# Performance work log

Measured on AMD Instinct MI355X. Metric: run time of the kernel, lower is better.

## Reference

```python
import jax, jax.numpy as jnp
import numpy as np

N_LABELS = 2048
N_CLASSES = 2
BATCH = 2048
BRANCH = 4


def _tree():
    # deterministic rooted tree: parent(i) = (i-1)//BRANCH, node 0 is root
    parent = np.full(N_LABELS, -1, dtype=np.int64)
    parent[1:] = (np.arange(1, N_LABELS) - 1) // BRANCH
    depth = np.zeros(N_LABELS, dtype=np.int64)
    for i in range(1, N_LABELS):
        depth[i] = depth[parent[i]] + 1
    levels = [np.where(depth == d)[0] for d in range(int(depth.max()) + 1)]
    return parent, levels

_PARENT, _LEVELS = _tree()  # static structure (from the adjacency init arg)


def setup_inputs() -> dict:
    key = jax.random.key(0)
    k1, k2 = jax.random.split(key)
    emissions = jax.random.normal(k1, (BATCH, N_CLASSES, N_LABELS), dtype=jnp.float32)
    pairs = jax.random.normal(k2, (N_LABELS, N_LABELS, N_CLASSES, N_CLASSES), dtype=jnp.float32)
    return {"emissions": emissions, "pairs": pairs}


def _messages(emissions, pairs, upward):
    """Belief-propagation messages, level-synchronous (topological order).

    upward=True  -> alphas: messages from children to parents (leaves->root)
    upward=False -> betas:  messages from parents to children (root->leaves)
    """
    B, C, L = emissions.shape
    acc = jnp.zeros((B, C, L), emissions.dtype)
    if upward:
        # process deepest level first; all nodes at level d send to their
        # (level d-1) parents; duplicate parent indices accumulate via .add
        for d in range(len(_LEVELS) - 1, 0, -1):
            nodes = _LEVELS[d]      # senders (children), (K,)
            par = _PARENT[nodes]    # receivers (parents), (K,)
            # local[b, k, yc] = emissions[b, yc, node_k] + acc[b, yc, node_k]
            local = (emissions[:, :, nodes] + acc[:, :, nodes]).transpose(0, 2, 1)
            trans = pairs[par, nodes]  # (K, Cp, Cc): pairs[parent, child]
            # msg[b, k, yp] = logsumexp_yc( trans[k, yp, yc] + local[b, k, yc] )
            msg = jax.nn.logsumexp(trans[None] + local[:, :, None, :], axis=-1)
            acc = acc.at[:, :, par].add(msg.transpose(0, 2, 1))
    else:
        # process shallow -> deep; each node receives from its parent,
        # whose betas were completed in the previous level iteration
        for d in range(1, len(_LEVELS)):
            nodes = _LEVELS[d]      # receivers (children)
            par = _PARENT[nodes]    # senders (parents)
            local = (emissions[:, :, par] + acc[:, :, par]).transpose(0, 2, 1)  # (B,K,Cp)
            trans = pairs[nodes, par]  # (K, Cc, Cp): pairs[child, parent]
            msg = jax.nn.logsumexp(trans[None] + local[:, :, None, :], axis=-1)  # (B,K,Cc)
            acc = acc.at[:, :, nodes].add(msg.transpose(0, 2, 1))
    return acc


def reference(emissions, pairs):
    alphas = _messages(emissions, pairs, True)
    betas = _messages(emissions, pairs, False)
    scores = emissions + alphas + betas  # (B, C, L)
    # normalize over classes per label -> log marginals log p(y_i | X)
    return scores - jax.nn.logsumexp(scores, axis=1, keepdims=True)
```

## Files before the change

### kernel.cpp

```cpp
#include <hip/hip_runtime.h>


constexpr int NLAB = 2048;
constexpr int NBATCH = 2048;

#define LOG2E 1.4426950408889634f
#define LN2   0.6931471805599453f

__device__ __forceinline__ float fexp2(float x) { return __builtin_amdgcn_exp2f(x); }
__device__ __forceinline__ float flog2(float x) { return __builtin_amdgcn_logf(x); }

__global__ __launch_bounds__(256) void compact_pairs(
    const float4* __restrict__ pairs4,
    float4* __restrict__ up,
    float4* __restrict__ down)
{
    int i = blockIdx.x * 256 + threadIdx.x;
    if (i < NLAB - 1) {
        int c = i + 1, p = i >> 2;
        float4 t = pairs4[(size_t)p * NLAB + c];
        up[i] = make_float4(t.x, t.z,
                            fexp2((t.y - t.x) * LOG2E),
                            fexp2((t.w - t.z) * LOG2E));
        float4 s = pairs4[(size_t)c * NLAB + p];
        down[i] = make_float4(s.x, s.z,
                              fexp2((s.y - s.x) * LOG2E),
                              fexp2((s.w - s.z) * LOG2E));
    }
}

__global__ __launch_bounds__(256) void treecrf_kernel(
    const float* __restrict__ em_g,
    const float4* __restrict__ up,
    const float4* __restrict__ down,
    float* __restrict__ out)
{
    __shared__ float em[2 * NLAB];
    __shared__ float al[2 * NLAB];

    const int b = blockIdx.x;
    const int tid = threadIdx.x;
    const float* __restrict__ eb = em_g + (size_t)b * 2 * NLAB;

    for (int l2 = tid; l2 < NLAB / 2; l2 += 256) {
        float2 e0 = reinterpret_cast<const float2*>(eb)[l2];
        float2 e1 = reinterpret_cast<const float2*>(eb + NLAB)[l2];
        reinterpret_cast<float4*>(em)[l2] = make_float4(e0.x, e1.x, e0.y, e1.y);
        reinterpret_cast<float4*>(al)[l2] = make_float4(0.f, 0.f, 0.f, 0.f);
    }
    __syncthreads();

    const int ustart[6] = {1364, 340, 84, 20, 4, 0};
    const int uend[6]   = {2048, 1364, 340, 84, 20, 4};
#pragma unroll
    for (int pass = 0; pass < 6; ++pass) {
        for (int i = ustart[pass] + tid; i < uend[pass]; i += 256) {
            const bool valid = (i + 1) < NLAB;
            const int c = valid ? i + 1 : NLAB - 1;
            float2 e = reinterpret_cast<const float2*>(em)[c];
            float l0 = e.x, l1 = e.y;
            if (pass > 0) {
                float2 a = reinterpret_cast<const float2*>(al)[c];
                l0 += a.x; l1 += a.y;
            }
            float4 t = up[min(i, NLAB - 2)];
            float eu = fexp2((l1 - l0) * LOG2E);
            float m0 = t.x + l0 + LN2 * flog2(fmaf(eu, t.z, 1.f));
            float m1 = t.y + l0 + LN2 * flog2(fmaf(eu, t.w, 1.f));
            if (!valid) { m0 = 0.f; m1 = 0.f; }
            m0 += __shfl_xor(m0, 1, 4);  m0 += __shfl_xor(m0, 2, 4);
            m1 += __shfl_xor(m1, 1, 4);  m1 += __shfl_xor(m1, 2, 4);
            if ((i & 3) == 0)
                reinterpret_cast<float2*>(al)[i >> 2] = make_float2(m0, m1);
        }
        __syncthreads();
    }

    float* __restrict__ ob0 = out + (size_t)b * 2 * NLAB;
    float* __restrict__ ob1 = ob0 + NLAB;

    if (tid == 0) {
        float s0 = em[0] + al[0];
        float s1 = em[1] + al[1];
        float Z = s0 + LN2 * flog2(1.f + fexp2((s1 - s0) * LOG2E));
        ob0[0] = s0 - Z;
        ob1[0] = s1 - Z;
    }
    __syncthreads();

    const int dstart[6] = {1, 5, 21, 85, 341, 1365};
    const int dend[6]   = {5, 21, 85, 341, 1365, 2048};
#pragma unroll
    for (int pass = 0; pass < 6; ++pass) {
        for (int n = dstart[pass] + tid; n < dend[pass]; n += 256) {
            const int par = (n - 1) >> 2;
            float2 pp = reinterpret_cast<const float2*>(em)[par];
            float4 t = down[n - 1];
            float eu = fexp2((pp.y - pp.x) * LOG2E);
            float m0 = t.x + pp.x + LN2 * flog2(fmaf(eu, t.z, 1.f));
            float m1 = t.y + pp.x + LN2 * flog2(fmaf(eu, t.w, 1.f));
            float pb0 = em[n * 2 + 0] + m0;
            float pb1 = em[n * 2 + 1] + m1;
            em[n * 2 + 0] = pb0;
            em[n * 2 + 1] = pb1;
            float s0 = pb0 + al[n * 2 + 0];
            float s1 = pb1 + al[n * 2 + 1];
            float Z = s0 + LN2 * flog2(1.f + fexp2((s1 - s0) * LOG2E));
            ob0[n] = s0 - Z;
            ob1[n] = s1 - Z;
        }
        __syncthreads();
    }
}

extern "C" void kernel_launch(void* const* d_in, const int* in_sizes, int n_in,
                              void* d_out, int out_size, void* d_ws, size_t ws_size,
                              hipStream_t stream) {
    const float*  emissions = (const float*)d_in[0];
    const float4* pairs4    = (const float4*)d_in[1];
    float* outp             = (float*)d_out;

    float4* upw = (float4*)d_ws;
    float4* dnw = upw + (NLAB - 1);
    compact_pairs<<<dim3((NLAB + 255) / 256), dim3(256), 0, stream>>>(pairs4, upw, dnw);
    treecrf_kernel<<<dim3(NBATCH), dim3(256), 0, stream>>>(emissions, upw, dnw, outp);
}
```

Before: 133.9 us.

## Use single-wavefront blocks per batch row and drop barriers and shared emission copy

Each batch row is now handled by one 64-lane wavefront instead of 256 threads, so all __syncthreads barriers between tree levels are removed. Emissions are read straight from global memory instead of being staged in LDS, and shared memory shrinks to internal-node alphas only (first 512 labels), with that buffer reused for the downward parent beliefs. This cuts LDS footprint and barrier cost and allows more resident blocks, at the price of less parallelism per row and uncoalesced-ish global reads. Correctness relies on wavefront lockstep ordering of LDS writes and reads within a wave.

```diff
diff --git a/kernel.cpp b/kernel.cpp
--- a/kernel.cpp
+++ b/kernel.cpp
@@ -29,39 +29,34 @@
     }
 }
 
-__global__ __launch_bounds__(256) void treecrf_kernel(
+__global__ __launch_bounds__(64) void treecrf_kernel(
     const float* __restrict__ em_g,
     const float4* __restrict__ up,
     const float4* __restrict__ down,
     float* __restrict__ out)
 {
-    __shared__ float em[2 * NLAB];
-    __shared__ float al[2 * NLAB];
+    __shared__ float al[2 * 512];
+    float2* al2 = reinterpret_cast<float2*>(al);
 
     const int b = blockIdx.x;
-    const int tid = threadIdx.x;
-    const float* __restrict__ eb = em_g + (size_t)b * 2 * NLAB;
-
-    for (int l2 = tid; l2 < NLAB / 2; l2 += 256) {
-        float2 e0 = reinterpret_cast<const float2*>(eb)[l2];
-        float2 e1 = reinterpret_cast<const float2*>(eb + NLAB)[l2];
-        reinterpret_cast<float4*>(em)[l2] = make_float4(e0.x, e1.x, e0.y, e1.y);
-        reinterpret_cast<float4*>(al)[l2] = make_float4(0.f, 0.f, 0.f, 0.f);
-    }
-    __syncthreads();
+    const int lane = threadIdx.x;
+    const float* __restrict__ e0g = em_g + (size_t)b * 2 * NLAB;
+    const float* __restrict__ e1g = e0g + NLAB;
 
     const int ustart[6] = {1364, 340, 84, 20, 4, 0};
     const int uend[6]   = {2048, 1364, 340, 84, 20, 4};
 #pragma unroll
     for (int pass = 0; pass < 6; ++pass) {
-        for (int i = ustart[pass] + tid; i < uend[pass]; i += 256) {
+        for (int i = ustart[pass] + lane; i < uend[pass]; i += 64) {
             const bool valid = (i + 1) < NLAB;
             const int c = valid ? i + 1 : NLAB - 1;
-            float2 e = reinterpret_cast<const float2*>(em)[c];
-            float l0 = e.x, l1 = e.y;
+            float l0 = e0g[c];
+            float l1 = e1g[c];
             if (pass > 0) {
-                float2 a = reinterpret_cast<const float2*>(al)[c];
-                l0 += a.x; l1 += a.y;
+                float2 a = al2[min(c, 511)];
+                bool internal = c < 512;
+                l0 += internal ? a.x : 0.f;
+                l1 += internal ? a.y : 0.f;
             }
             float4 t = up[min(i, NLAB - 2)];
             float eu = fexp2((l1 - l0) * LOG2E);
@@ -71,45 +66,50 @@
             m0 += __shfl_xor(m0, 1, 4);  m0 += __shfl_xor(m0, 2, 4);
             m1 += __shfl_xor(m1, 1, 4);  m1 += __shfl_xor(m1, 2, 4);
             if ((i & 3) == 0)
-                reinterpret_cast<float2*>(al)[i >> 2] = make_float2(m0, m1);
+                al2[i >> 2] = make_float2(m0, m1);
         }
-        __syncthreads();
     }
 
     float* __restrict__ ob0 = out + (size_t)b * 2 * NLAB;
     float* __restrict__ ob1 = ob0 + NLAB;
 
-    if (tid == 0) {
-        float s0 = em[0] + al[0];
-        float s1 = em[1] + al[1];
+    if (lane == 0) {
+        float pb0 = e0g[0];
+        float pb1 = e1g[0];
+        float s0 = pb0 + al[0];
+        float s1 = pb1 + al[1];
         float Z = s0 + LN2 * flog2(1.f + fexp2((s1 - s0) * LOG2E));
         ob0[0] = s0 - Z;
         ob1[0] = s1 - Z;
+        al2[0] = make_float2(pb0, pb1);
     }
-    __syncthreads();
 
     const int dstart[6] = {1, 5, 21, 85, 341, 1365};
     const int dend[6]   = {5, 21, 85, 341, 1365, 2048};
 #pragma unroll
     for (int pass = 0; pass < 6; ++pass) {
-        for (int n = dstart[pass] + tid; n < dend[pass]; n += 256) {
+        for (int n = dstart[pass] + lane; n < dend[pass]; n += 64) {
             const int par = (n - 1) >> 2;
-            float2 pp = reinterpret_cast<const float2*>(em)[par];
+            float2 pp = al2[par];
             float4 t = down[n - 1];
             float eu = fexp2((pp.y - pp.x) * LOG2E);
             float m0 = t.x + pp.x + LN2 * flog2(fmaf(eu, t.z, 1.f));
             float m1 = t.y + pp.x + LN2 * flog2(fmaf(eu, t.w, 1.f));
-            float pb0 = em[n * 2 + 0] + m0;
-            float pb1 = em[n * 2 + 1] + m1;
-            em[n * 2 + 0] = pb0;
-            em[n * 2 + 1] = pb1;
-            float s0 = pb0 + al[n * 2 + 0];
-            float s1 = pb1 + al[n * 2 + 1];
+            float a0 = 0.f, a1 = 0.f;
+            if (pass < 5) {
+                float2 a = al2[min(n, 511)];
+                if (n < 512) { a0 = a.x; a1 = a.y; }
+            }
+            float pb0 = e0g[n] + m0;
+            float pb1 = e1g[n] + m1;
+            if (pass < 5 && n < 512)
+                al2[n] = make_float2(pb0, pb1);
+            float s0 = pb0 + a0;
+            float s1 = pb1 + a1;
             float Z = s0 + LN2 * flog2(1.f + fexp2((s1 - s0) * LOG2E));
             ob0[n] = s0 - Z;
             ob1[n] = s1 - Z;
         }
-        __syncthreads();
     }
 }
 
@@ -123,5 +123,5 @@
     float4* upw = (float4*)d_ws;
     float4* dnw = upw + (NLAB - 1);
     compact_pairs<<<dim3((NLAB + 255) / 256), dim3(256), 0, stream>>>(pairs4, upw, dnw);
-    treecrf_kernel<<<dim3(NBATCH), dim3(256), 0, stream>>>(emissions, upw, dnw, outp);
+    treecrf_kernel<<<dim3(NBATCH), dim3(64), 0, stream>>>(emissions, upw, dnw, outp);
 }
```

After: 149.8 us. 11.9% more time.
